# Performance work log

Hardware: AMD Instinct MI355X
Metric: run time of the kernel (lower is better)

## Reference

```python
import jax, jax.numpy as jnp
import numpy as np

# Production-scale dims (see shape_source)
N = 100000      # nodes
E = 1600000     # shortest-path edges
I = 128         # in_channels
O = 128         # out_channels
K = 5           # max_distance
BN_EPS = 1e-5
GIN_EPS = 0.0   # eps=0.0, trainable_eps=False


def setup_inputs() -> dict:
    key = jax.random.key(0)
    ks = jax.random.split(key, 10)
    node_embeddings = jax.random.normal(ks[0], (N, I), dtype=jnp.float32)
    edge_index = jax.random.randint(ks[1], (2, E), 0, N)          # [2, E] row/col
    edge_weights = jax.random.randint(ks[2], (E,), 1, K + 1)      # SP distance in 1..K
    hop_coef = jax.random.normal(ks[3], (K,), dtype=jnp.float32)
    W1 = jax.random.normal(ks[4], (I, O), dtype=jnp.float32) / np.sqrt(I).astype(np.float32)
    b1 = jnp.zeros((O,), jnp.float32)
    gamma1 = jnp.ones((O,), jnp.float32)
    beta1 = jnp.zeros((O,), jnp.float32)
    W2 = jax.random.normal(ks[5], (O, O), dtype=jnp.float32) / np.sqrt(O).astype(np.float32)
    b2 = jnp.zeros((O,), jnp.float32)
    gamma2 = jnp.ones((O,), jnp.float32)
    beta2 = jnp.zeros((O,), jnp.float32)
    return {
        "node_embeddings": node_embeddings,
        "edge_index": edge_index,
        "edge_weights": edge_weights,
        "hop_coef": hop_coef,
        "W1": W1, "b1": b1, "gamma1": gamma1, "beta1": beta1,
        "W2": W2, "b2": b2, "gamma2": gamma2, "beta2": beta2,
    }


def _batch_norm(x, gamma, beta):
    # BatchNorm1d in training mode: batch mean, biased batch variance
    mean = x.mean(axis=0)
    var = x.var(axis=0)
    return gamma * (x - mean) * jax.lax.rsqrt(var + BN_EPS) + beta


def reference(node_embeddings, edge_index, edge_weights, hop_coef,
              W1, b1, gamma1, beta1, W2, b2, gamma2, beta2):
    # Fused form of the per-hop loop: each edge with SP distance d contributes
    # softmax(hop_coef)[d-1] * x[col] to out[row]. Identical math to K separate
    # sparse.mm's weighted by hop_weights and summed.
    hop_w = jax.nn.softmax(hop_coef)                               # [K]
    valid = (edge_weights >= 1) & (edge_weights <= K)
    w_e = jnp.where(valid, hop_w[jnp.clip(edge_weights - 1, 0, K - 1)], 0.0)  # [E]
    row, col = edge_index[0], edge_index[1]
    msgs = w_e[:, None] * node_embeddings[col]                     # [E, I] gather
    agg = jnp.zeros_like(node_embeddings).at[row].add(msgs)        # [N, I] scatter-add
    h = (1.0 + GIN_EPS) * node_embeddings + agg                    # GIN combine
    h = jax.nn.relu(_batch_norm(h @ W1 + b1, gamma1, beta1))
    h = jax.nn.relu(_batch_norm(h @ W2 + b2, gamma2, beta2))
    return h
```

## Files before the change

kernel.cpp:

```cpp
#include <hip/hip_runtime.h>
#include <hip/hip_bf16.h>


#define RCAP 64
#define P2B 256
#define BPB 4

typedef __attribute__((ext_vector_type(8))) short short8;
typedef __attribute__((ext_vector_type(4))) float f32x4;

__device__ inline unsigned short f2bf(float v) {
    unsigned int u = __float_as_uint(v);
    return (unsigned short)((u + 0x7fffu + ((u >> 16) & 1u)) >> 16);
}
__device__ inline float bf2f(unsigned int u) { return __uint_as_float(u << 16); }
__device__ inline float bflo(unsigned int u) { return __uint_as_float(u << 16); }
__device__ inline float bfhi(unsigned int u) { return __uint_as_float(u & 0xFFFF0000u); }

__global__ __launch_bounds__(256) void prep_k(
        const float* __restrict__ hc, float* __restrict__ hwp, float* __restrict__ sums,
        const float* __restrict__ W1, const float* __restrict__ W2,
        unsigned short* __restrict__ w1h, unsigned short* __restrict__ w1l,
        unsigned short* __restrict__ w2h, unsigned short* __restrict__ w2l,
        const float4* __restrict__ x4, uint4* __restrict__ xb, int K, long long n8,
        const int* __restrict__ rows, int* __restrict__ C, int* __restrict__ cur,
        int E, int per, int nbukp, int N, int NX) {
    __shared__ int hist[128];
    int b = blockIdx.x, tid = threadIdx.x;
    if (b == 0) {
        sums[tid] = 0.f; sums[tid + 256] = 0.f;
        if (tid == 0) {
            float tmp[8];
            float m = -1e30f;
            for (int k = 0; k < K; ++k) m = fmaxf(m, hc[k]);
            float s = 0.f;
            for (int k = 0; k < K; ++k) { float e = __expf(hc[k] - m); tmp[k] = e; s += e; }
            float inv = 1.f / s;
            for (int k = 0; k < 8; ++k) hwp[k] = 0.f;
            for (int k = 0; k < K; ++k) hwp[k + 1] = tmp[k] * inv;
        }
        return;
    }
    if (b <= 2) {
        const float* W = (b == 2) ? W2 : W1;
        unsigned short* th = (b == 2) ? w2h : w1h;
        unsigned short* tl = (b == 2) ? w2l : w1l;
        for (int i = tid; i < 16384; i += 256) {
            int k = i >> 7, n = i & 127;
            float v = W[k * 128 + n];
            unsigned short hi = f2bf(v);
            th[n * 128 + k] = hi;
            tl[n * 128 + k] = f2bf(v - bf2f(hi));
        }
        return;
    }
    if (b < 3 + NX) {
        long long g = (long long)(b - 3) * 256 + tid;
        if (g >= n8) return;
        float4 a = x4[g * 2], c = x4[g * 2 + 1];
        union { unsigned short us[8]; uint4 v; } o;
        o.us[0] = f2bf(a.x); o.us[1] = f2bf(a.y); o.us[2] = f2bf(a.z); o.us[3] = f2bf(a.w);
        o.us[4] = f2bf(c.x); o.us[5] = f2bf(c.y); o.us[6] = f2bf(c.z); o.us[7] = f2bf(c.w);
        xb[g] = o.v;
        return;
    }
    int cblk = b - 3 - NX;
    for (int i = tid; i < nbukp; i += 256) hist[i] = 0;
    __syncthreads();
    int e0 = cblk * per, e1 = min(E, e0 + per);
    for (int e = e0 + tid; e < e1; e += 256)
        atomicAdd(&hist[rows[e] >> 10], 1);
    __syncthreads();
    for (int i = tid; i < nbukp; i += 256) C[i * P2B + cblk] = hist[i];
    int zper = (N + P2B - 1) / P2B;
    int z0 = cblk * zper, z1 = min(N, z0 + zper);
    for (int i = z0 + tid; i < z1; i += 256) cur[i] = 0;
}

__global__ __launch_bounds__(256) void scan1_k(int* __restrict__ C,
        int* __restrict__ tot, int nbukp, int nblk) {
    __shared__ int buf[256];
    int b = blockIdx.x, tid = threadIdx.x;
    int v = (tid < nblk) ? C[b * P2B + tid] : 0;
    buf[tid] = v;
    __syncthreads();
#pragma unroll
    for (int off = 1; off < 256; off <<= 1) {
        int t = (tid >= off) ? buf[tid - off] : 0;
        __syncthreads();
        buf[tid] += t;
        __syncthreads();
    }
    if (tid < nblk) C[b * P2B + tid] = buf[tid] - v;
    if (tid == 255) tot[b] = buf[255];
}

__global__ __launch_bounds__(256) void scatter_k(const int* __restrict__ rows,
        const int* __restrict__ cols, const int* __restrict__ ew,
        const int* __restrict__ O, const int* __restrict__ tot,
        unsigned* __restrict__ bucketed, int E, int per, int nbukp, int K) {
    __shared__ int buf[128];
    __shared__ unsigned curs[128];
    int blk = blockIdx.x, tid = threadIdx.x;
    int v = (tid < 128 && tid < nbukp) ? tot[tid] : 0;
    if (tid < 128) buf[tid] = v;
    __syncthreads();
#pragma unroll
    for (int off = 1; off < 128; off <<= 1) {
        int t = (tid >= off && tid < 128) ? buf[tid - off] : 0;
        __syncthreads();
        if (tid < 128) buf[tid] += t;
        __syncthreads();
    }
    if (tid < nbukp)
        curs[tid] = (unsigned)(O[tid * P2B + blk] + buf[tid] - v);
    __syncthreads();
    int e0 = blk * per, e1 = min(E, e0 + per);
    for (int e = e0 + tid; e < e1; e += 256) {
        int r = rows[e];
        int c = cols[e];
        int d = ew[e];
        if (d < 1 || d > K) d = 0;
        unsigned idx = atomicAdd(&curs[r >> 10], 1u);
        bucketed[idx] = (unsigned)d | ((unsigned)c << 3) | ((unsigned)(r & 1023) << 20);
    }
}

__global__ __launch_bounds__(256) void slot3_k(const unsigned* __restrict__ bucketed,
        const int* __restrict__ tot, int* __restrict__ cur,
        unsigned* __restrict__ staging, int nbukp) {
    __shared__ int buf[128];
    int tid = threadIdx.x;
    if (tid < 128) buf[tid] = (tid < nbukp) ? tot[tid] : 0;
    __syncthreads();
#pragma unroll
    for (int off = 1; off < 128; off <<= 1) {
        int t = (tid >= off && tid < 128) ? buf[tid - off] : 0;
        __syncthreads();
        if (tid < 128) buf[tid] += t;
        __syncthreads();
    }
    int bucket = blockIdx.x % nbukp, sub = blockIdx.x / nbukp;
    int s1 = buf[bucket];
    int s0 = s1 - tot[bucket];
    int cnt = s1 - s0;
    int qlo = s0 + (int)((long long)cnt * sub / BPB);
    int qhi = s0 + (int)((long long)cnt * (sub + 1) / BPB);
    int rbase = bucket << 10;
    for (int e = qlo + tid; e < qhi; e += 256) {
        unsigned u = bucketed[e];
        int row = rbase + (int)(u >> 20);
        int s = atomicAdd(&cur[row], 1);
        if (s < RCAP)
            staging[((size_t)row << 6) + s] = u & 0xFFFFFu;
    }
}

__global__ __launch_bounds__(256) void slot_k(const int* __restrict__ rows,
        const int* __restrict__ cols, const int* __restrict__ ew,
        int* __restrict__ cur, unsigned* __restrict__ staging, int E, int K) {
    int e = blockIdx.x * 256 + threadIdx.x;
    if (e >= E) return;
    int r = rows[e];
    int d = ew[e];
    if (d < 1 || d > K) d = 0;
    int s = atomicAdd(&cur[r], 1);
    if (s < RCAP)
        staging[((size_t)r << 6) + s] = (unsigned)d | ((unsigned)cols[e] << 3);
}

__global__ __launch_bounds__(256) void gather_k(
        const unsigned short* __restrict__ xb, const unsigned* __restrict__ staging,
        const int* __restrict__ cur, const float* __restrict__ hwp,
        unsigned short* __restrict__ h, int N) {
    __shared__ float hwl[8];
    int tid = threadIdx.x;
    if (tid < 8) hwl[tid] = hwp[tid];
    __syncthreads();
    int wid = (blockIdx.x * 256 + tid) >> 6;
    if (wid >= N) return;
    int lane = tid & 63;
    int g4 = lane >> 4, li = lane & 15;
    int deg = __builtin_amdgcn_readfirstlane(cur[wid]);
    deg = min(deg, RCAP);
    const unsigned* ep = staging + ((size_t)wid << 6);
    const unsigned short* xrow = xb + li * 8;
    float a0 = 0.f, a1 = 0.f, a2 = 0.f, a3 = 0.f;
    float a4 = 0.f, a5 = 0.f, a6 = 0.f, a7 = 0.f;
    if (g4 == 0) {
        uint4 u = *(const uint4*)(xb + (size_t)wid * 128 + li * 8);
        a0 = bflo(u.x); a1 = bfhi(u.x); a2 = bflo(u.y); a3 = bfhi(u.y);
        a4 = bflo(u.z); a5 = bfhi(u.z); a6 = bflo(u.w); a7 = bfhi(u.w);
    }
    int j = 0;
    for (; j + 16 <= deg; j += 16) {
        unsigned p0 = ep[j + g4];
        unsigned p1 = ep[j + 4 + g4];
        unsigned p2 = ep[j + 8 + g4];
        unsigned p3 = ep[j + 12 + g4];
        uint4 u0 = *(const uint4*)(xrow + (size_t)(p0 >> 3) * 128);
        uint4 u1 = *(const uint4*)(xrow + (size_t)(p1 >> 3) * 128);
        uint4 u2 = *(const uint4*)(xrow + (size_t)(p2 >> 3) * 128);
        uint4 u3 = *(const uint4*)(xrow + (size_t)(p3 >> 3) * 128);
        float w0 = hwl[p0 & 7], w1 = hwl[p1 & 7];
        float w2 = hwl[p2 & 7], w3 = hwl[p3 & 7];
        a0 = fmaf(w0, bflo(u0.x), a0); a1 = fmaf(w0, bfhi(u0.x), a1);
        a2 = fmaf(w0, bflo(u0.y), a2); a3 = fmaf(w0, bfhi(u0.y), a3);
        a4 = fmaf(w0, bflo(u0.z), a4); a5 = fmaf(w0, bfhi(u0.z), a5);
        a6 = fmaf(w0, bflo(u0.w), a6); a7 = fmaf(w0, bfhi(u0.w), a7);
        a0 = fmaf(w1, bflo(u1.x), a0); a1 = fmaf(w1, bfhi(u1.x), a1);
        a2 = fmaf(w1, bflo(u1.y), a2); a3 = fmaf(w1, bfhi(u1.y), a3);
        a4 = fmaf(w1, bflo(u1.z), a4); a5 = fmaf(w1, bfhi(u1.z), a5);
        a6 = fmaf(w1, bflo(u1.w), a6); a7 = fmaf(w1, bfhi(u1.w), a7);
        a0 = fmaf(w2, bflo(u2.x), a0); a1 = fmaf(w2, bfhi(u2.x), a1);
        a2 = fmaf(w2, bflo(u2.y), a2); a3 = fmaf(w2, bfhi(u2.y), a3);
        a4 = fmaf(w2, bflo(u2.z), a4); a5 = fmaf(w2, bfhi(u2.z), a5);
        a6 = fmaf(w2, bflo(u2.w), a6); a7 = fmaf(w2, bfhi(u2.w), a7);
        a0 = fmaf(w3, bflo(u3.x), a0); a1 = fmaf(w3, bfhi(u3.x), a1);
        a2 = fmaf(w3, bflo(u3.y), a2); a3 = fmaf(w3, bfhi(u3.y), a3);
        a4 = fmaf(w3, bflo(u3.z), a4); a5 = fmaf(w3, bfhi(u3.z), a5);
        a6 = fmaf(w3, bflo(u3.w), a6); a7 = fmaf(w3, bfhi(u3.w), a7);
    }
    for (; j + 4 <= deg; j += 4) {
        unsigned p = ep[j + g4];
        uint4 u = *(const uint4*)(xrow + (size_t)(p >> 3) * 128);
        float w = hwl[p & 7];
        a0 = fmaf(w, bflo(u.x), a0); a1 = fmaf(w, bfhi(u.x), a1);
        a2 = fmaf(w, bflo(u.y), a2); a3 = fmaf(w, bfhi(u.y), a3);
        a4 = fmaf(w, bflo(u.z), a4); a5 = fmaf(w, bfhi(u.z), a5);
        a6 = fmaf(w, bflo(u.w), a6); a7 = fmaf(w, bfhi(u.w), a7);
    }
    if (j < deg) {
        int jj = min(j + g4, deg - 1);
        unsigned p = ep[jj];
        float w = (j + g4 < deg) ? hwl[p & 7] : 0.f;
        uint4 u = *(const uint4*)(xrow + (size_t)(p >> 3) * 128);
        a0 = fmaf(w, bflo(u.x), a0); a1 = fmaf(w, bfhi(u.x), a1);
        a2 = fmaf(w, bflo(u.y), a2); a3 = fmaf(w, bfhi(u.y), a3);
        a4 = fmaf(w, bflo(u.z), a4); a5 = fmaf(w, bfhi(u.z), a5);
        a6 = fmaf(w, bflo(u.w), a6); a7 = fmaf(w, bfhi(u.w), a7);
    }
    a0 += __shfl_xor(a0, 16); a1 += __shfl_xor(a1, 16);
    a2 += __shfl_xor(a2, 16); a3 += __shfl_xor(a3, 16);
    a4 += __shfl_xor(a4, 16); a5 += __shfl_xor(a5, 16);
    a6 += __shfl_xor(a6, 16); a7 += __shfl_xor(a7, 16);
    a0 += __shfl_xor(a0, 32); a1 += __shfl_xor(a1, 32);
    a2 += __shfl_xor(a2, 32); a3 += __shfl_xor(a3, 32);
    a4 += __shfl_xor(a4, 32); a5 += __shfl_xor(a5, 32);
    a6 += __shfl_xor(a6, 32); a7 += __shfl_xor(a7, 32);
    if (g4 == 0) {
        uint4 o;
        o.x = (unsigned int)f2bf(a0) | ((unsigned int)f2bf(a1) << 16);
        o.y = (unsigned int)f2bf(a2) | ((unsigned int)f2bf(a3) << 16);
        o.z = (unsigned int)f2bf(a4) | ((unsigned int)f2bf(a5) << 16);
        o.w = (unsigned int)f2bf(a6) | ((unsigned int)f2bf(a7) << 16);
        *(uint4*)(h + (size_t)wid * 128 + li * 8) = o;
    }
}

__global__ __launch_bounds__(256, 4) void gemm_mfma_k(
        const unsigned short* __restrict__ Ain,
        const unsigned short* __restrict__ Bhg, const unsigned short* __restrict__ Blg,
        const float* __restrict__ bias, unsigned short* __restrict__ zout,
        float* __restrict__ sum_out, float* __restrict__ sq_out, int N) {
    __shared__ unsigned short Bs[128 * 136];
    int tid = threadIdx.x;
    int wave = tid >> 6, lane = tid & 63;
    int n16 = lane & 15, q = lane >> 4;
    int rowbase = blockIdx.x * 128 + wave * 32;
    for (int i = tid; i < 2048; i += 256) {
        int n = i >> 4, c = i & 15;
        *(uint4*)&Bs[n * 136 + c * 8] = *(const uint4*)(Bhg + n * 128 + c * 8);
    }
    short8 afr[4][2];
#pragma unroll
    for (int kk = 0; kk < 4; kk++)
#pragma unroll
        for (int mt = 0; mt < 2; mt++) {
            int ar = rowbase + mt * 16 + n16;
            ar = min(ar, N - 1);
            afr[kk][mt] = *(const short8*)(Ain + (size_t)ar * 128 + kk * 32 + q * 8);
        }
    f32x4 acc[2][8];
#pragma unroll
    for (int mt = 0; mt < 2; mt++)
#pragma unroll
        for (int t = 0; t < 8; t++) acc[mt][t] = (f32x4){0.f, 0.f, 0.f, 0.f};
    __syncthreads();
    int ldsb = n16 * 136 + q * 8;
#pragma unroll
    for (int kk = 0; kk < 4; kk++)
#pragma unroll
        for (int t = 0; t < 8; t++) {
            short8 b = *(const short8*)&Bs[t * 16 * 136 + ldsb + kk * 32];
            acc[0][t] = __builtin_amdgcn_mfma_f32_16x16x32_bf16(afr[kk][0], b, acc[0][t], 0, 0, 0);
            acc[1][t] = __builtin_amdgcn_mfma_f32_16x16x32_bf16(afr[kk][1], b, acc[1][t], 0, 0, 0);
        }
    __syncthreads();
    for (int i = tid; i < 2048; i += 256) {
        int n = i >> 4, c = i & 15;
        *(uint4*)&Bs[n * 136 + c * 8] = *(const uint4*)(Blg + n * 128 + c * 8);
    }
    __syncthreads();
#pragma unroll
    for (int kk = 0; kk < 4; kk++)
#pragma unroll
        for (int t = 0; t < 8; t++) {
            short8 b = *(const short8*)&Bs[t * 16 * 136 + ldsb + kk * 32];
            acc[0][t] = __builtin_amdgcn_mfma_f32_16x16x32_bf16(afr[kk][0], b, acc[0][t], 0, 0, 0);
            acc[1][t] = __builtin_amdgcn_mfma_f32_16x16x32_bf16(afr[kk][1], b, acc[1][t], 0, 0, 0);
        }
    float csum[8], csq[8];
#pragma unroll
    for (int t = 0; t < 8; t++) { csum[t] = 0.f; csq[t] = 0.f; }
#pragma unroll
    for (int t = 0; t < 8; t++) {
        int col = n16 + 16 * t;
        float bv = bias[col];
#pragma unroll
        for (int mt = 0; mt < 2; mt++) {
#pragma unroll
            for (int r = 0; r < 4; r++) {
                int row = rowbase + mt * 16 + q * 4 + r;
                if (row < N) {
                    float v = acc[mt][t][r] + bv;
                    zout[(size_t)row * 128 + col] = f2bf(v);
                    csum[t] += v;
                    csq[t] += v * v;
                }
            }
        }
    }
#pragma unroll
    for (int t = 0; t < 8; t++) {
        csum[t] += __shfl_xor(csum[t], 16);
        csum[t] += __shfl_xor(csum[t], 32);
        csq[t] += __shfl_xor(csq[t], 16);
        csq[t] += __shfl_xor(csq[t], 32);
    }
    __syncthreads();
    float* red = (float*)Bs;
    if (q == 0) {
#pragma unroll
        for (int t = 0; t < 8; t++) {
            int col = n16 + 16 * t;
            red[wave * 128 + col] = csum[t];
            red[512 + wave * 128 + col] = csq[t];
        }
    }
    __syncthreads();
    if (tid < 128) {
        float s = 0.f, qq = 0.f;
#pragma unroll
        for (int w = 0; w < 4; w++) {
            s += red[w * 128 + tid];
            qq += red[512 + w * 128 + tid];
        }
        unsafeAtomicAdd(&sum_out[tid], s);
        unsafeAtomicAdd(&sq_out[tid], qq);
    }
}

__global__ __launch_bounds__(256, 4) void gemm_mfma_bn_k(
        const unsigned short* __restrict__ Zin,
        const float* __restrict__ sum_in, const float* __restrict__ sq_in,
        const float* __restrict__ gamma, const float* __restrict__ beta,
        float invN,
        const unsigned short* __restrict__ Bhg, const unsigned short* __restrict__ Blg,
        const float* __restrict__ bias, unsigned short* __restrict__ zout,
        float* __restrict__ sum_out, float* __restrict__ sq_out, int N) {
    __shared__ unsigned short Bs[128 * 136];
    __shared__ float sc[128], sh[128];
    int tid = threadIdx.x;
    int wave = tid >> 6, lane = tid & 63;
    int n16 = lane & 15, q = lane >> 4;
    int rowbase = blockIdx.x * 128 + wave * 32;
    for (int i = tid; i < 2048; i += 256) {
        int n = i >> 4, c = i & 15;
        *(uint4*)&Bs[n * 136 + c * 8] = *(const uint4*)(Bhg + n * 128 + c * 8);
    }
    if (tid < 128) {
        float mean = sum_in[tid] * invN;
        float var = fmaxf(sq_in[tid] * invN - mean * mean, 0.f);
        float s = gamma[tid] * rsqrtf(var + 1e-5f);
        sc[tid] = s;
        sh[tid] = beta[tid] - mean * s;
    }
    __syncthreads();
    short8 afr[4][2];
#pragma unroll
    for (int kk = 0; kk < 4; kk++)
#pragma unroll
        for (int mt = 0; mt < 2; mt++) {
            int ar = rowbase + mt * 16 + n16;
            ar = min(ar, N - 1);
            short8 raw = *(const short8*)(Zin + (size_t)ar * 128 + kk * 32 + q * 8);
            short8 outv;
#pragma unroll
            for (int i = 0; i < 8; i++) {
                int col = kk * 32 + q * 8 + i;
                float f = bf2f((unsigned short)raw[i]);
                float v = fmaxf(fmaf(f, sc[col], sh[col]), 0.f);
                outv[i] = (short)f2bf(v);
            }
            afr[kk][mt] = outv;
        }
    f32x4 acc[2][8];
#pragma unroll
    for (int mt = 0; mt < 2; mt++)
#pragma unroll
        for (int t = 0; t < 8; t++) acc[mt][t] = (f32x4){0.f, 0.f, 0.f, 0.f};
    int ldsb = n16 * 136 + q * 8;
#pragma unroll
    for (int kk = 0; kk < 4; kk++)
#pragma unroll
        for (int t = 0; t < 8; t++) {
            short8 b = *(const short8*)&Bs[t * 16 * 136 + ldsb + kk * 32];
            acc[0][t] = __builtin_amdgcn_mfma_f32_16x16x32_bf16(afr[kk][0], b, acc[0][t], 0, 0, 0);
            acc[1][t] = __builtin_amdgcn_mfma_f32_16x16x32_bf16(afr[kk][1], b, acc[1][t], 0, 0, 0);
        }
    __syncthreads();
    for (int i = tid; i < 2048; i += 256) {
        int n = i >> 4, c = i & 15;
        *(uint4*)&Bs[n * 136 + c * 8] = *(const uint4*)(Blg + n * 128 + c * 8);
    }
    __syncthreads();
#pragma unroll
    for (int kk = 0; kk < 4; kk++)
#pragma unroll
        for (int t = 0; t < 8; t++) {
            short8 b = *(const short8*)&Bs[t * 16 * 136 + ldsb + kk * 32];
            acc[0][t] = __builtin_amdgcn_mfma_f32_16x16x32_bf16(afr[kk][0], b, acc[0][t], 0, 0, 0);
            acc[1][t] = __builtin_amdgcn_mfma_f32_16x16x32_bf16(afr[kk][1], b, acc[1][t], 0, 0, 0);
        }
    float csum[8], csq[8];
#pragma unroll
    for (int t = 0; t < 8; t++) { csum[t] = 0.f; csq[t] = 0.f; }
#pragma unroll
    for (int t = 0; t < 8; t++) {
        int col = n16 + 16 * t;
        float bv = bias[col];
#pragma unroll
        for (int mt = 0; mt < 2; mt++) {
#pragma unroll
            for (int r = 0; r < 4; r++) {
                int row = rowbase + mt * 16 + q * 4 + r;
                if (row < N) {
                    float v = acc[mt][t][r] + bv;
                    zout[(size_t)row * 128 + col] = f2bf(v);
                    csum[t] += v;
                    csq[t] += v * v;
                }
            }
        }
    }
#pragma unroll
    for (int t = 0; t < 8; t++) {
        csum[t] += __shfl_xor(csum[t], 16);
        csum[t] += __shfl_xor(csum[t], 32);
        csq[t] += __shfl_xor(csq[t], 16);
        csq[t] += __shfl_xor(csq[t], 32);
    }
    __syncthreads();
    float* red = (float*)Bs;
    if (q == 0) {
#pragma unroll
        for (int t = 0; t < 8; t++) {
            int col = n16 + 16 * t;
            red[wave * 128 + col] = csum[t];
            red[512 + wave * 128 + col] = csq[t];
        }
    }
    __syncthreads();
    if (tid < 128) {
        float s = 0.f, qq = 0.f;
#pragma unroll
        for (int w = 0; w < 4; w++) {
            s += red[w * 128 + tid];
            qq += red[512 + w * 128 + tid];
        }
        unsafeAtomicAdd(&sum_out[tid], s);
        unsafeAtomicAdd(&sq_out[tid], qq);
    }
}

__global__ __launch_bounds__(256) void bn2_k(const unsigned short* __restrict__ z2,
        const float* __restrict__ sum2, const float* __restrict__ sq2,
        const float* __restrict__ gamma, const float* __restrict__ beta,
        float* __restrict__ out, long long n8, float invN) {
    __shared__ float sc[128], sh[128];
    int tid = threadIdx.x;
    if (tid < 128) {
        float mean = sum2[tid] * invN;
        float var = fmaxf(sq2[tid] * invN - mean * mean, 0.f);
        float s = gamma[tid] * rsqrtf(var + 1e-5f);
        sc[tid] = s;
        sh[tid] = beta[tid] - mean * s;
    }
    __syncthreads();
    long long g = (long long)blockIdx.x * 256 + tid;
    if (g >= n8) return;
    uint4 u = ((const uint4*)z2)[g];
    int cb = (int)((g * 8) & 127);
    float4 s0 = *(const float4*)&sc[cb], s1 = *(const float4*)&sc[cb + 4];
    float4 t0 = *(const float4*)&sh[cb], t1 = *(const float4*)&sh[cb + 4];
    float4 o0, o1;
    o0.x = fmaxf(fmaf(bflo(u.x), s0.x, t0.x), 0.f);
    o0.y = fmaxf(fmaf(bfhi(u.x), s0.y, t0.y), 0.f);
    o0.z = fmaxf(fmaf(bflo(u.y), s0.z, t0.z), 0.f);
    o0.w = fmaxf(fmaf(bfhi(u.y), s0.w, t0.w), 0.f);
    o1.x = fmaxf(fmaf(bflo(u.z), s1.x, t1.x), 0.f);
    o1.y = fmaxf(fmaf(bfhi(u.z), s1.y, t1.y), 0.f);
    o1.z = fmaxf(fmaf(bflo(u.w), s1.z, t1.z), 0.f);
    o1.w = fmaxf(fmaf(bfhi(u.w), s1.w, t1.w), 0.f);
    ((float4*)out)[g * 2] = o0;
    ((float4*)out)[g * 2 + 1] = o1;
}

extern "C" void kernel_launch(void* const* d_in, const int* in_sizes, int n_in,
                              void* d_out, int out_size, void* d_ws, size_t ws_size,
                              hipStream_t stream) {
    const float* x   = (const float*)d_in[0];
    const int*   ei  = (const int*)d_in[1];
    const int*   ew  = (const int*)d_in[2];
    const float* hc  = (const float*)d_in[3];
    const float* W1  = (const float*)d_in[4];
    const float* b1  = (const float*)d_in[5];
    const float* g1  = (const float*)d_in[6];
    const float* be1 = (const float*)d_in[7];
    const float* W2  = (const float*)d_in[8];
    const float* b2  = (const float*)d_in[9];
    const float* g2  = (const float*)d_in[10];
    const float* be2 = (const float*)d_in[11];

    int N = in_sizes[0] / 128;
    int E = in_sizes[2];
    int K = in_sizes[3];
    size_t NF = (size_t)N * 128;
    long long n8 = (long long)(NF / 8);
    int NX = (int)((n8 + 255) / 256);

    unsigned short* h = (unsigned short*)d_ws;
    unsigned short* xb = h + NF;
    unsigned short* z1 = xb;
    unsigned short* z2 = h;
    unsigned* staging = (unsigned*)(xb + NF);
    int* cur = (int*)(staging + (size_t)N * RCAP);
    unsigned short* w1h = (unsigned short*)(cur + N);
    unsigned short* w1l = w1h + 16384;
    unsigned short* w2h = w1l + 16384;
    unsigned short* w2l = w2h + 16384;
    float* hwp = (float*)(w2l + 16384);
    float* sums = hwp + 8;
    float* sum1 = sums, *sq1 = sums + 128, *sum2 = sums + 256, *sq2 = sums + 384;
    int nbuk  = (N + 1023) >> 10;
    int nbukp = (nbuk + 7) & ~7;
    int* C = (int*)(sums + 512);
    int* tot = C + (size_t)nbukp * P2B;
    unsigned* bucketed = (unsigned*)(tot + nbukp);
    size_t ws_need = (size_t)((char*)(bucketed + E) - (char*)d_ws);
    bool use_bucketed = (nbukp <= 128) && (N <= (1 << 17)) && (K <= 7)
                        && (ws_need <= ws_size);

    float invN = 1.0f / (float)N;
    int per = (E + P2B - 1) / P2B;

    int prep_grid = use_bucketed ? (3 + NX + P2B) : (3 + NX);
    if (!use_bucketed)
        hipMemsetAsync(cur, 0, (size_t)N * sizeof(int), stream);
    prep_k<<<prep_grid, 256, 0, stream>>>(hc, hwp, sums, W1, W2,
        w1h, w1l, w2h, w2l, (const float4*)x, (uint4*)xb, K, n8,
        ei, C, cur, E, per, nbukp, N, NX);
    if (use_bucketed) {
        scan1_k<<<nbukp, 256, 0, stream>>>(C, tot, nbukp, P2B);
        scatter_k<<<P2B, 256, 0, stream>>>(ei, ei + E, ew, C, tot, bucketed,
                                           E, per, nbukp, K);
        slot3_k<<<nbukp * BPB, 256, 0, stream>>>(bucketed, tot, cur, staging, nbukp);
    } else {
        slot_k<<<(E + 255) / 256, 256, 0, stream>>>(ei, ei + E, ew, cur, staging, E, K);
    }
    {
        long long tot_thr = (long long)N * 64;
        gather_k<<<(int)((tot_thr + 255) / 256), 256, 0, stream>>>(
            xb, staging, cur, hwp, h, N);
    }
    int gblocks = (N + 127) / 128;
    gemm_mfma_k<<<gblocks, 256, 0, stream>>>(h, w1h, w1l, b1, z1, sum1, sq1, N);
    gemm_mfma_bn_k<<<gblocks, 256, 0, stream>>>(z1, sum1, sq1, g1, be1, invN,
        w2h, w2l, b2, z2, sum2, sq2, N);
    bn2_k<<<NX, 256, 0, stream>>>(z2, sum2, sq2, g2, be2, (float*)d_out, n8, invN);
}
```

Before: 422.7 us.

## Replace fixed-capacity per-row staging with a compact CSR built by in-bucket counting sort

The third sort pass now performs a full counting sort inside each 1024-row bucket using shared-memory histograms and prefix scans. It emits a compact CSR (rowstart plus rowsorted) instead of scattering edges into fixed 64-slot per-row staging through global atomics on cur. The gather kernel reads contiguous neighbor lists, and per-row zeroing of cur in prep goes away. This removes global atomics and the RCAP truncation, and makes the edge reads dense. The cost is that the pass runs one block per bucket (about 98 blocks) instead of four per bucket, which lowers parallelism.

```diff
diff --git a/kernel.cpp b/kernel.cpp
--- a/kernel.cpp
+++ b/kernel.cpp
@@ -4,7 +4,6 @@
 
 #define RCAP 64
 #define P2B 256
-#define BPB 4
 
 typedef __attribute__((ext_vector_type(8))) short short8;
 typedef __attribute__((ext_vector_type(4))) float f32x4;
@@ -23,7 +22,7 @@
         unsigned short* __restrict__ w1h, unsigned short* __restrict__ w1l,
         unsigned short* __restrict__ w2h, unsigned short* __restrict__ w2l,
         const float4* __restrict__ x4, uint4* __restrict__ xb, int K, long long n8,
-        const int* __restrict__ rows, int* __restrict__ C, int* __restrict__ cur,
+        const int* __restrict__ rows, int* __restrict__ C,
         int E, int per, int nbukp, int N, int NX) {
     __shared__ int hist[128];
     int b = blockIdx.x, tid = threadIdx.x;
@@ -72,9 +71,6 @@
         atomicAdd(&hist[rows[e] >> 10], 1);
     __syncthreads();
     for (int i = tid; i < nbukp; i += 256) C[i * P2B + cblk] = hist[i];
-    int zper = (N + P2B - 1) / P2B;
-    int z0 = cblk * zper, z1 = min(N, z0 + zper);
-    for (int i = z0 + tid; i < z1; i += 256) cur[i] = 0;
 }
 
 __global__ __launch_bounds__(256) void scan1_k(int* __restrict__ C,
@@ -126,33 +122,62 @@
     }
 }
 
-__global__ __launch_bounds__(256) void slot3_k(const unsigned* __restrict__ bucketed,
-        const int* __restrict__ tot, int* __restrict__ cur,
-        unsigned* __restrict__ staging, int nbukp) {
-    __shared__ int buf[128];
+__global__ __launch_bounds__(256) void slot3s_k(const unsigned* __restrict__ bucketed,
+        const int* __restrict__ tot, unsigned* __restrict__ rowsorted,
+        int* __restrict__ rowstart, int nbukp, int N) {
+    __shared__ int bbuf[128];
+    __shared__ int cnt[1024];
+    __shared__ int pre[1024];
+    __shared__ int sb[256];
     int tid = threadIdx.x;
-    if (tid < 128) buf[tid] = (tid < nbukp) ? tot[tid] : 0;
+    if (tid < 128) bbuf[tid] = (tid < nbukp) ? tot[tid] : 0;
     __syncthreads();
 #pragma unroll
     for (int off = 1; off < 128; off <<= 1) {
-        int t = (tid >= off && tid < 128) ? buf[tid - off] : 0;
-        __syncthreads();
-        if (tid < 128) buf[tid] += t;
-        __syncthreads();
-    }
-    int bucket = blockIdx.x % nbukp, sub = blockIdx.x / nbukp;
-    int s1 = buf[bucket];
-    int s0 = s1 - tot[bucket];
-    int cnt = s1 - s0;
-    int qlo = s0 + (int)((long long)cnt * sub / BPB);
-    int qhi = s0 + (int)((long long)cnt * (sub + 1) / BPB);
+        int t = (tid >= off && tid < 128) ? bbuf[tid - off] : 0;
+        __syncthreads();
+        if (tid < 128) bbuf[tid] += t;
+        __syncthreads();
+    }
+    int bucket = blockIdx.x;
+    int s1 = bbuf[bucket];
+    int cntb = tot[bucket];
+    int s0 = s1 - cntb;
     int rbase = bucket << 10;
-    for (int e = qlo + tid; e < qhi; e += 256) {
+    int rlim = min(1024, N - rbase);
+    if (bucket == 0 && tid == 0) rowstart[N] = bbuf[127];
+    for (int i = tid; i < 1024; i += 256) cnt[i] = 0;
+    __syncthreads();
+    for (int e = s0 + tid; e < s1; e += 256)
+        atomicAdd(&cnt[bucketed[e] >> 20], 1);
+    __syncthreads();
+    int b4 = tid * 4;
+    int c0 = cnt[b4], c1 = cnt[b4 + 1], c2 = cnt[b4 + 2], c3 = cnt[b4 + 3];
+    int ts = c0 + c1 + c2 + c3;
+    sb[tid] = ts;
+    __syncthreads();
+#pragma unroll
+    for (int off = 1; off < 256; off <<= 1) {
+        int t = (tid >= off) ? sb[tid - off] : 0;
+        __syncthreads();
+        sb[tid] += t;
+        __syncthreads();
+    }
+    int eb = sb[tid] - ts;
+    pre[b4] = eb;
+    pre[b4 + 1] = eb + c0;
+    pre[b4 + 2] = eb + c0 + c1;
+    pre[b4 + 3] = eb + c0 + c1 + c2;
+    __syncthreads();
+    for (int lr = tid; lr < rlim; lr += 256)
+        rowstart[rbase + lr] = s0 + pre[lr];
+    for (int i = tid; i < 1024; i += 256) cnt[i] = pre[i];
+    __syncthreads();
+    for (int e = s0 + tid; e < s1; e += 256) {
         unsigned u = bucketed[e];
-        int row = rbase + (int)(u >> 20);
-        int s = atomicAdd(&cur[row], 1);
-        if (s < RCAP)
-            staging[((size_t)row << 6) + s] = u & 0xFFFFFu;
+        int lr = (int)(u >> 20);
+        int p = atomicAdd(&cnt[lr], 1);
+        rowsorted[s0 + p] = u & 0xFFFFFu;
     }
 }
 
@@ -170,8 +195,8 @@
 }
 
 __global__ __launch_bounds__(256) void gather_k(
-        const unsigned short* __restrict__ xb, const unsigned* __restrict__ staging,
-        const int* __restrict__ cur, const float* __restrict__ hwp,
+        const unsigned short* __restrict__ xb, const unsigned* __restrict__ rowsorted,
+        const int* __restrict__ rowstart, const float* __restrict__ hwp,
         unsigned short* __restrict__ h, int N) {
     __shared__ float hwl[8];
     int tid = threadIdx.x;
@@ -181,9 +206,9 @@
     if (wid >= N) return;
     int lane = tid & 63;
     int g4 = lane >> 4, li = lane & 15;
-    int deg = __builtin_amdgcn_readfirstlane(cur[wid]);
-    deg = min(deg, RCAP);
-    const unsigned* ep = staging + ((size_t)wid << 6);
+    int st = rowstart[wid];
+    int deg = rowstart[wid + 1] - st;
+    const unsigned* ep = rowsorted + st;
     const unsigned short* xrow = xb + li * 8;
     float a0 = 0.f, a1 = 0.f, a2 = 0.f, a3 = 0.f;
     float a4 = 0.f, a5 = 0.f, a6 = 0.f, a7 = 0.f;
@@ -258,6 +283,57 @@
     }
 }
 
+__global__ __launch_bounds__(256) void gather_stg_k(
+        const unsigned short* __restrict__ xb, const unsigned* __restrict__ staging,
+        const int* __restrict__ cur, const float* __restrict__ hwp,
+        unsigned short* __restrict__ h, int N) {
+    __shared__ float hwl[8];
+    int tid = threadIdx.x;
+    if (tid < 8) hwl[tid] = hwp[tid];
+    __syncthreads();
+    int wid = (blockIdx.x * 256 + tid) >> 6;
+    if (wid >= N) return;
+    int lane = tid & 63;
+    int g4 = lane >> 4, li = lane & 15;
+    int deg = __builtin_amdgcn_readfirstlane(cur[wid]);
+    deg = min(deg, RCAP);
+    const unsigned* ep = staging + ((size_t)wid << 6);
+    const unsigned short* xrow = xb + li * 8;
+    float a0 = 0.f, a1 = 0.f, a2 = 0.f, a3 = 0.f;
+    float a4 = 0.f, a5 = 0.f, a6 = 0.f, a7 = 0.f;
+    if (g4 == 0) {
+        uint4 u = *(const uint4*)(xb + (size_t)wid * 128 + li * 8);
+        a0 = bflo(u.x); a1 = bfhi(u.x); a2 = bflo(u.y); a3 = bfhi(u.y);
+        a4 = bflo(u.z); a5 = bfhi(u.z); a6 = bflo(u.w); a7 = bfhi(u.w);
+    }
+    for (int j = 0; j < deg; j += 4) {
+        int jj = min(j + g4, deg - 1);
+        unsigned p = ep[jj];
+        float w = (j + g4 < deg) ? hwl[p & 7] : 0.f;
+        uint4 u = *(const uint4*)(xrow + (size_t)(p >> 3) * 128);
+        a0 = fmaf(w, bflo(u.x), a0); a1 = fmaf(w, bfhi(u.x), a1);
+        a2 = fmaf(w, bflo(u.y), a2); a3 = fmaf(w, bfhi(u.y), a3);
+        a4 = fmaf(w, bflo(u.z), a4); a5 = fmaf(w, bfhi(u.z), a5);
+        a6 = fmaf(w, bflo(u.w), a6); a7 = fmaf(w, bfhi(u.w), a7);
+    }
+    a0 += __shfl_xor(a0, 16); a1 += __shfl_xor(a1, 16);
+    a2 += __shfl_xor(a2, 16); a3 += __shfl_xor(a3, 16);
+    a4 += __shfl_xor(a4, 16); a5 += __shfl_xor(a5, 16);
+    a6 += __shfl_xor(a6, 16); a7 += __shfl_xor(a7, 16);
+    a0 += __shfl_xor(a0, 32); a1 += __shfl_xor(a1, 32);
+    a2 += __shfl_xor(a2, 32); a3 += __shfl_xor(a3, 32);
+    a4 += __shfl_xor(a4, 32); a5 += __shfl_xor(a5, 32);
+    a6 += __shfl_xor(a6, 32); a7 += __shfl_xor(a7, 32);
+    if (g4 == 0) {
+        uint4 o;
+        o.x = (unsigned int)f2bf(a0) | ((unsigned int)f2bf(a1) << 16);
+        o.y = (unsigned int)f2bf(a2) | ((unsigned int)f2bf(a3) << 16);
+        o.z = (unsigned int)f2bf(a4) | ((unsigned int)f2bf(a5) << 16);
+        o.w = (unsigned int)f2bf(a6) | ((unsigned int)f2bf(a7) << 16);
+        *(uint4*)(h + (size_t)wid * 128 + li * 8) = o;
+    }
+}
+
 __global__ __launch_bounds__(256, 4) void gemm_mfma_k(
         const unsigned short* __restrict__ Ain,
         const unsigned short* __restrict__ Bhg, const unsigned short* __restrict__ Blg,
@@ -545,6 +621,7 @@
     unsigned short* z1 = xb;
     unsigned short* z2 = h;
     unsigned* staging = (unsigned*)(xb + NF);
+    unsigned* rowsorted = staging;
     int* cur = (int*)(staging + (size_t)N * RCAP);
     unsigned short* w1h = (unsigned short*)(cur + N);
     unsigned short* w1l = w1h + 16384;
@@ -558,8 +635,10 @@
     int* C = (int*)(sums + 512);
     int* tot = C + (size_t)nbukp * P2B;
     unsigned* bucketed = (unsigned*)(tot + nbukp);
-    size_t ws_need = (size_t)((char*)(bucketed + E) - (char*)d_ws);
+    int* rowstart = (int*)(bucketed + E);
+    size_t ws_need = (size_t)((char*)(rowstart + N + 1) - (char*)d_ws);
     bool use_bucketed = (nbukp <= 128) && (N <= (1 << 17)) && (K <= 7)
+                        && ((size_t)E <= (size_t)N * RCAP)
                         && (ws_need <= ws_size);
 
     float invN = 1.0f / (float)N;
@@ -570,19 +649,19 @@
         hipMemsetAsync(cur, 0, (size_t)N * sizeof(int), stream);
     prep_k<<<prep_grid, 256, 0, stream>>>(hc, hwp, sums, W1, W2,
         w1h, w1l, w2h, w2l, (const float4*)x, (uint4*)xb, K, n8,
-        ei, C, cur, E, per, nbukp, N, NX);
+        ei, C, E, per, nbukp, N, NX);
+    long long tot_thr = (long long)N * 64;
+    int ggrid = (int)((tot_thr + 255) / 256);
     if (use_bucketed) {
         scan1_k<<<nbukp, 256, 0, stream>>>(C, tot, nbukp, P2B);
         scatter_k<<<P2B, 256, 0, stream>>>(ei, ei + E, ew, C, tot, bucketed,
                                            E, per, nbukp, K);
-        slot3_k<<<nbukp * BPB, 256, 0, stream>>>(bucketed, tot, cur, staging, nbukp);
+        slot3s_k<<<nbukp, 256, 0, stream>>>(bucketed, tot, rowsorted, rowstart,
+                                            nbukp, N);
+        gather_k<<<ggrid, 256, 0, stream>>>(xb, rowsorted, rowstart, hwp, h, N);
     } else {
         slot_k<<<(E + 255) / 256, 256, 0, stream>>>(ei, ei + E, ew, cur, staging, E, K);
-    }
-    {
-        long long tot_thr = (long long)N * 64;
-        gather_k<<<(int)((tot_thr + 255) / 256), 256, 0, stream>>>(
-            xb, staging, cur, hwp, h, N);
+        gather_stg_k<<<ggrid, 256, 0, stream>>>(xb, staging, cur, hwp, h, N);
     }
     int gblocks = (N + 127) / 128;
     gemm_mfma_k<<<gblocks, 256, 0, stream>>>(h, w1h, w1l, b1, z1, sum1, sq1, N);
```

New measurement: 409.2 us. 3.2% less time.
